# Optimization experiments

Hardware: AMD Instinct MI355X
Metric: run time of the kernel (lower is better)

Reference implementation:

```python
import jax, jax.numpy as jnp
import numpy as np

B, T, C = 8, 4096, 192
HIMG, WIMG = 64, 64
NH, HS = 24, 8
MIX_DIM, DECAY_DIM = 32, 64


def _conv2d(x, w, pad):
    # x: [B, C, H, W], w: [Cout, Cin, kh, kw]
    return jax.lax.conv_general_dilated(
        x, w, (1, 1), [(pad, pad), (pad, pad)],
        dimension_numbers=('NCHW', 'OIHW', 'NCHW'))


def setup_inputs() -> dict:
    key = jax.random.key(0)
    ks = jax.random.split(key, 26)
    f = jax.random.normal
    s = 1.0 / np.sqrt(C)
    return {
        'x': f(ks[0], (B, T, C), jnp.float32),
        'maa_x': f(ks[1], (1, 1, C), jnp.float32) * 0.1,
        'maa_w': f(ks[2], (1, 1, C), jnp.float32) * 0.1,
        'maa_k': f(ks[3], (1, 1, C), jnp.float32) * 0.1,
        'maa_v': f(ks[4], (1, 1, C), jnp.float32) * 0.1,
        'maa_r': f(ks[5], (1, 1, C), jnp.float32) * 0.1,
        'maa_g': f(ks[6], (1, 1, C), jnp.float32) * 0.1,
        'maa_w1': f(ks[7], (C, 5 * MIX_DIM), jnp.float32) * 0.01,
        'maa_w2': f(ks[8], (5, MIX_DIM, C), jnp.float32) * 0.01,
        'decay_w1': f(ks[9], (C, DECAY_DIM), jnp.float32) * 0.01,
        'decay_w2': f(ks[10], (DECAY_DIM, C), jnp.float32) * 0.01,
        'spatial_decay': f(ks[11], (1, 1, C), jnp.float32) * 0.5,
        'u': f(ks[12], (NH, HS), jnp.float32) * 0.5,
        'Wr': f(ks[13], (C, C), jnp.float32) * s,
        'Wk': f(ks[14], (C, C), jnp.float32) * s,
        'Wv': f(ks[15], (C, C), jnp.float32) * s,
        'Wg': f(ks[16], (C, C), jnp.float32) * s,
        'Wo': f(ks[17], (C, C), jnp.float32) * s,
        'ln_g': jnp.ones((C,), jnp.float32),
        'ln_b': jnp.zeros((C,), jnp.float32),
        'w_lp': f(ks[18], (C, C), jnp.float32) * s,
        'w_hd': f(ks[19], (C, C, 3), jnp.float32) * s,
        'w_vd': f(ks[20], (C, C, 3), jnp.float32) * s,
        'w_cd': f(ks[21], (C, C, 3, 3), jnp.float32) * (s / 3.0),
        'theta_cd': jnp.full((1,), 0.7, jnp.float32),
    }


def _diff_conv_mix(x2d, w_lp, w_hd, w_vd, w_cd, theta_cd):
    Cc = x2d.shape[1]
    # laplacian-pattern conv from a 1x1 weight (Conv2d_lp)
    k9 = jnp.zeros((Cc, Cc, 9), x2d.dtype)
    k9 = k9.at[:, :, jnp.array([1, 3, 5, 7])].set(w_lp[:, :, None])
    k9 = k9.at[:, :, 4].set(-4.0 * w_lp)
    out = _conv2d(x2d, k9.reshape(Cc, Cc, 3, 3), 1)
    # horizontal difference conv (Conv2d_hd)
    k9 = jnp.zeros((Cc, Cc, 9), x2d.dtype)
    k9 = k9.at[:, :, jnp.array([0, 3, 6])].set(w_hd)
    k9 = k9.at[:, :, jnp.array([2, 5, 8])].set(-w_hd)
    out = out + _conv2d(x2d, k9.reshape(Cc, Cc, 3, 3), 1)
    # vertical difference conv (Conv2d_vd)
    k9 = jnp.zeros((Cc, Cc, 9), x2d.dtype)
    k9 = k9.at[:, :, jnp.array([0, 1, 2])].set(w_vd)
    k9 = k9.at[:, :, jnp.array([6, 7, 8])].set(-w_vd)
    out = out + _conv2d(x2d, k9.reshape(Cc, Cc, 3, 3), 1)
    # central difference conv (Conv2d_cd): normal conv + 1x1 (-theta * kernel sum)
    out = out + _conv2d(x2d, w_cd, 1)
    kd = jnp.sum(w_cd, axis=(2, 3), keepdims=True) * (-theta_cd[0])
    out = out + _conv2d(x2d, kd, 0)
    return out


def reference(x, maa_x, maa_w, maa_k, maa_v, maa_r, maa_g, maa_w1, maa_w2,
              decay_w1, decay_w2, spatial_decay, u, Wr, Wk, Wv, Wg, Wo,
              ln_g, ln_b, w_lp, w_hd, w_vd, w_cd, theta_cd):
    Bb, Tt, Cc = x.shape
    x2d = x.transpose(0, 2, 1).reshape(Bb, Cc, HIMG, WIMG)
    shifted = _diff_conv_mix(x2d, w_lp, w_hd, w_vd, w_cd, theta_cd)
    xx = shifted.reshape(Bb, Cc, Tt).transpose(0, 2, 1) - x  # spatial shift delta

    # data-dependent token mixing (RWKV6 maa)
    xxx = x + xx * maa_x
    tmp = jnp.tanh(xxx @ maa_w1).reshape(Bb, Tt, 5, MIX_DIM)
    m = jnp.einsum('btfd,fdc->fbtc', tmp, maa_w2)  # [5, B, T, C]
    mw, mk, mv, mr, mg = m[0], m[1], m[2], m[3], m[4]
    xw = x + xx * (maa_w + mw)
    xk = x + xx * (maa_k + mk)
    xv = x + xx * (maa_v + mv)
    xr = x + xx * (maa_r + mr)
    xg = x + xx * (maa_g + mg)

    r = xr @ Wr
    k = xk @ Wk
    v = xv @ Wv
    g = jax.nn.silu(xg @ Wg)
    w = spatial_decay + jnp.tanh(xw @ decay_w1) @ decay_w2  # [B, T, C]

    # WKV6 linear recurrence, fp32 state, per-head [HS, HS]
    rh = r.reshape(Bb, Tt, NH, HS).astype(jnp.float32)
    kh = k.reshape(Bb, Tt, NH, HS).astype(jnp.float32)
    vh = v.reshape(Bb, Tt, NH, HS).astype(jnp.float32)
    dh = jnp.exp(-jnp.exp(w.astype(jnp.float32))).reshape(Bb, Tt, NH, HS)
    uf = u.astype(jnp.float32)

    def step(S, inp):  # S: [B, NH, HS(j key), HS(i value)]
        rt, kt, vt, dt = inp  # each [B, NH, HS]
        kv = kt[..., :, None] * vt[..., None, :]
        yt = jnp.einsum('bhj,bhji->bhi', rt, S + uf[None, :, :, None] * kv)
        return dt[..., None] * S + kv, yt

    xs = tuple(a.transpose(1, 0, 2, 3) for a in (rh, kh, vh, dh))  # time-major
    S0 = jnp.zeros((Bb, NH, HS, HS), jnp.float32)
    _, ys = jax.lax.scan(step, S0, xs)
    y = ys.transpose(1, 0, 2, 3).reshape(Bb, Tt, Cc).astype(x.dtype)

    # ln_x then gated output projection
    mu = jnp.mean(y, axis=-1, keepdims=True)
    var = jnp.mean((y - mu) ** 2, axis=-1, keepdims=True)
    yn = (y - mu) * jax.lax.rsqrt(var + 1e-5) * ln_g + ln_b
    return (yn * g) @ Wo
```

## Files before the change

### kernel.cpp

```cpp
#include <hip/hip_runtime.h>
#include <hip/hip_bf16.h>

#define Bq 8
#define Tq 4096
#define Cq 192
#define NHq 24
#define HSq 8
#define Mq (Bq * Tq)

#define CLq 64
#define NCHq (Tq / CLq)
#define TSq 32

typedef short short8 __attribute__((ext_vector_type(8)));
typedef float f32x4 __attribute__((ext_vector_type(4)));

__device__ __forceinline__ unsigned short f2bf(float f) {
    union { float f; unsigned u; } v; v.f = f;
    unsigned u = v.u;
    return (unsigned short)((u + 0x7FFFu + ((u >> 16) & 1u)) >> 16);
}
__device__ __forceinline__ float bf2f(unsigned short u) {
    union { unsigned u; float f; } v; v.u = (unsigned)u << 16;
    return v.f;
}
__device__ __forceinline__ float4 bf4_to_f4(ushort4 u) {
    return make_float4(bf2f(u.x), bf2f(u.y), bf2f(u.z), bf2f(u.w));
}

__global__ void prep_weights_kernel(const float* __restrict__ w_lp,
                                    const float* __restrict__ w_hd,
                                    const float* __restrict__ w_vd,
                                    const float* __restrict__ w_cd,
                                    const float* __restrict__ theta,
                                    unsigned short* __restrict__ Wg) {
    int idx = blockIdx.x * 256 + threadIdx.x;
    if (idx >= Cq * Cq) return;
    int cout = idx / Cq, cin = idx - cout * Cq;
    float t9[9];
#pragma unroll
    for (int t = 0; t < 9; ++t) t9[t] = 0.f;
    float lp = w_lp[idx];
    t9[1] += lp; t9[3] += lp; t9[5] += lp; t9[7] += lp; t9[4] -= 4.f * lp;
    float h0 = w_hd[idx * 3 + 0], h1 = w_hd[idx * 3 + 1], h2 = w_hd[idx * 3 + 2];
    t9[0] += h0; t9[3] += h1; t9[6] += h2;
    t9[2] -= h0; t9[5] -= h1; t9[8] -= h2;
    float v0 = w_vd[idx * 3 + 0], v1 = w_vd[idx * 3 + 1], v2 = w_vd[idx * 3 + 2];
    t9[0] += v0; t9[1] += v1; t9[2] += v2;
    t9[6] -= v0; t9[7] -= v1; t9[8] -= v2;
    float sum = 0.f;
#pragma unroll
    for (int t = 0; t < 9; ++t) {
        float cdv = w_cd[idx * 9 + t];
        t9[t] += cdv; sum += cdv;
    }
    t9[4] -= theta[0] * sum;
#pragma unroll
    for (int t = 0; t < 9; ++t)
        Wg[(size_t)cout * 1728 + t * Cq + cin] = f2bf(t9[t]);
}

__global__ void wtrans_kernel(const float* __restrict__ W,
                              unsigned short* __restrict__ Wt, int K, int N) {
    int idx = blockIdx.x * 256 + threadIdx.x;
    if (idx >= N * K) return;
    int n = idx / K, k = idx - n * K;
    Wt[idx] = f2bf(W[(size_t)k * N + n]);
}

__global__ void w2t_kernel(const float* __restrict__ w2,
                           unsigned short* __restrict__ w2t) {
    int idx = blockIdx.x * 256 + threadIdx.x;
    if (idx >= 5 * 192 * 32) return;
    int f = idx / (192 * 32), rem = idx - f * 192 * 32;
    int n = rem >> 5, k = rem & 31;
    w2t[idx] = f2bf(w2[(size_t)(f * 32 + k) * Cq + n]);
}

__global__ __launch_bounds__(256) void halo_kernel(
    const float* __restrict__ x, unsigned short* __restrict__ xh) {
    int idx = blockIdx.x * 256 + threadIdx.x;
    int c4 = (idx % 48) * 4;
    int cell = idx / 48;
    int hx = cell % 66;
    int rest = cell / 66;
    int hy = rest % 66;
    int bb = rest / 66;
    ushort4 o = make_ushort4(0, 0, 0, 0);
    if (hy >= 1 && hy <= 64 && hx >= 1 && hx <= 64) {
        size_t g = ((size_t)(bb << 12) + (hy - 1) * 64 + (hx - 1)) * Cq + c4;
        float4 v = *(const float4*)&x[g];
        o = make_ushort4(f2bf(v.x), f2bf(v.y), f2bf(v.z), f2bf(v.w));
    }
    *(ushort4*)&xh[(size_t)cell * Cq + c4] = o;
}

#define GBM 128
#define GBN 64
#define GBK 64

template <int ALOAD, int EPI, int OBF16>
__global__ __launch_bounds__(256) void mgemm_kernel(
    const unsigned short* __restrict__ Asrc,
    const unsigned short* __restrict__ Wt,
    void* __restrict__ Cv, int N, int K,
    const float* __restrict__ aux0,
    const unsigned short* __restrict__ xh,
    unsigned short* __restrict__ C2) {
    __shared__ unsigned char lds[(GBM + GBN) * GBK * 2];
    unsigned char* Alds = lds;
    unsigned char* Blds = lds + GBM * GBK * 2;
    float* C = (float*)Cv;
    unsigned short* Cb = (unsigned short*)Cv;

    const int tid = threadIdx.x;
    const int wid = tid >> 6, lane = tid & 63;
    const int llo = lane & 15, lhi = lane >> 4;
    const int m0 = blockIdx.x * GBM, n0 = blockIdx.y * GBN;

    f32x4 acc[2][4];
#pragma unroll
    for (int a = 0; a < 2; ++a)
#pragma unroll
        for (int b = 0; b < 4; ++b) {
            f32x4 z = {0.f, 0.f, 0.f, 0.f};
            acc[a][b] = z;
        }

    for (int k0 = 0; k0 < K; k0 += GBK) {
        __syncthreads();
#pragma unroll
        for (int rep = 0; rep < 4; ++rep) {
            int c = tid + rep * 256;
            int row = c >> 3, kseg = c & 7;
            int m = m0 + row;
            short8 val;
            if (ALOAD == 3) {
                val = *(const short8*)&Asrc[(size_t)m * K + k0 + kseg * 8];
            } else {
                int tap = k0 / Cq;
                int cinb = k0 - tap * Cq;
                int t3 = tap / 3;
                int bb = m >> 12, pos = m & 4095;
                int hy = (pos >> 6) + t3;
                int hx = (pos & 63) + tap - t3 * 3;
                size_t g = ((size_t)bb * 4356 + hy * 66 + hx) * Cq + cinb + kseg * 8;
                val = *(const short8*)&Asrc[g];
            }
            *(short8*)(Alds + row * 128 + ((kseg * 16) ^ ((row & 7) << 4))) = val;
        }
#pragma unroll
        for (int rep = 0; rep < 2; ++rep) {
            int c = tid + rep * 256;
            int row = c >> 3, kseg = c & 7;
            int n = n0 + row;
            short8 val = {0, 0, 0, 0, 0, 0, 0, 0};
            if (n < N) val = *(const short8*)&Wt[(size_t)n * K + k0 + kseg * 8];
            *(short8*)(Blds + row * 128 + ((kseg * 16) ^ ((row & 7) << 4))) = val;
        }
        __syncthreads();
#pragma unroll
        for (int kc = 0; kc < 2; ++kc) {
            int kb = kc * 64 + lhi * 16;
            short8 af[2], bq[4];
#pragma unroll
            for (int mf = 0; mf < 2; ++mf) {
                int row = wid * 32 + mf * 16 + llo;
                af[mf] = *(const short8*)(Alds + row * 128 + (kb ^ ((row & 7) << 4)));
            }
#pragma unroll
            for (int nf = 0; nf < 4; ++nf) {
                int row = nf * 16 + llo;
                bq[nf] = *(const short8*)(Blds + row * 128 + (kb ^ ((row & 7) << 4)));
            }
#pragma unroll
            for (int mf = 0; mf < 2; ++mf)
#pragma unroll
                for (int nf = 0; nf < 4; ++nf)
                    acc[mf][nf] = __builtin_amdgcn_mfma_f32_16x16x32_bf16(
                        af[mf], bq[nf], acc[mf][nf], 0, 0, 0);
        }
    }
    if (EPI == 5) {
#pragma unroll
        for (int mf = 0; mf < 2; ++mf)
#pragma unroll
            for (int nf = 0; nf < 4; ++nf) {
                int n = n0 + nf * 16 + llo;
#pragma unroll
                for (int r = 0; r < 4; ++r) {
                    int m = m0 + wid * 32 + mf * 16 + lhi * 4 + r;
                    int pos = m & 4095, bb = m >> 12;
                    size_t cell = (size_t)bb * 4356 + ((pos >> 6) + 1) * 66 + (pos & 63) + 1;
                    float xv = bf2f(xh[cell * Cq + n]);
                    float xxv = acc[mf][nf][r] - xv;
                    Cb[(size_t)m * Cq + n] = f2bf(xxv);
                    C2[(size_t)m * Cq + n] = f2bf(fmaf(xxv, aux0[n], xv));
                }
            }
        return;
    }
#pragma unroll
    for (int mf = 0; mf < 2; ++mf) {
#pragma unroll
        for (int nf = 0; nf < 4; ++nf) {
            int n = n0 + nf * 16 + llo;
            if (n >= N) continue;
#pragma unroll
            for (int r = 0; r < 4; ++r) {
                int m = m0 + wid * 32 + mf * 16 + lhi * 4 + r;
                float val = acc[mf][nf][r];
                if (EPI == 2) val = tanhf(val);
                else if (EPI == 3) val = val / (1.f + expf(-val));
                else if (EPI == 4) val = expf(-expf(aux0[n] + val));
                if (OBF16) Cb[(size_t)m * N + n] = f2bf(val);
                else C[(size_t)m * N + n] = val;
            }
        }
    }
}

__global__ __launch_bounds__(128) void mix5_kernel(
    const unsigned short* __restrict__ xh,
    const unsigned short* __restrict__ xxb,
    const unsigned short* __restrict__ tmp_bf,
    const unsigned short* __restrict__ w2t,
    const float* __restrict__ maa_w, const float* __restrict__ maa_k,
    const float* __restrict__ maa_v, const float* __restrict__ maa_r,
    const float* __restrict__ maa_g,
    unsigned short* __restrict__ xw, unsigned short* __restrict__ xr,
    unsigned short* __restrict__ xk, unsigned short* __restrict__ xv,
    unsigned short* __restrict__ xg) {
    const int tid = threadIdx.x;
    const int wid = tid >> 6, lane = tid & 63;
    const int llo = lane & 15, lhi = lane >> 4;
    const int mb = blockIdx.x * 64 + wid * 32;
    const int nb = blockIdx.y * 64;

    short8 aw[5][4];
#pragma unroll
    for (int f = 0; f < 5; ++f)
#pragma unroll
        for (int nf = 0; nf < 4; ++nf)
            aw[f][nf] = *(const short8*)&w2t[((size_t)f * Cq + nb + nf * 16 + llo) * 32 + lhi * 8];

#pragma unroll
    for (int sub = 0; sub < 2; ++sub) {
        short8 bt[5];
        {
            const unsigned short* trow = &tmp_bf[(size_t)(mb + sub * 16 + llo) * 160 + lhi * 8];
#pragma unroll
            for (int f = 0; f < 5; ++f) bt[f] = *(const short8*)&trow[f * 32];
        }
        int m = mb + sub * 16 + llo;
        int pos = m & 4095, bb = m >> 12;
        size_t xbase = ((size_t)bb * 4356 + ((pos >> 6) + 1) * 66 + (pos & 63) + 1) * Cq;
#pragma unroll
        for (int nf = 0; nf < 4; ++nf) {
            f32x4 acc[5];
#pragma unroll
            for (int f = 0; f < 5; ++f) {
                f32x4 z = {0.f, 0.f, 0.f, 0.f};
                acc[f] = __builtin_amdgcn_mfma_f32_16x16x32_bf16(aw[f][nf], bt[f], z, 0, 0, 0);
            }
            int n0 = nb + nf * 16 + lhi * 4;
            size_t g = (size_t)m * Cq + n0;
            float4 xv4 = bf4_to_f4(*(const ushort4*)&xh[xbase + n0]);
            float4 xx4 = bf4_to_f4(*(const ushort4*)&xxb[g]);
            float4 mw4 = *(const float4*)&maa_w[n0];
            float4 mk4 = *(const float4*)&maa_k[n0];
            float4 mv4 = *(const float4*)&maa_v[n0];
            float4 mr4 = *(const float4*)&maa_r[n0];
            float4 mg4 = *(const float4*)&maa_g[n0];
            float xvv[4] = {xv4.x, xv4.y, xv4.z, xv4.w};
            float xxv[4] = {xx4.x, xx4.y, xx4.z, xx4.w};
            float mwv[4] = {mw4.x, mw4.y, mw4.z, mw4.w};
            float mkv[4] = {mk4.x, mk4.y, mk4.z, mk4.w};
            float mvv[4] = {mv4.x, mv4.y, mv4.z, mv4.w};
            float mrv[4] = {mr4.x, mr4.y, mr4.z, mr4.w};
            float mgv[4] = {mg4.x, mg4.y, mg4.z, mg4.w};
            ushort4 ow, ok, ov, orr, og;
            unsigned short* owp = (unsigned short*)&ow;
            unsigned short* okp = (unsigned short*)&ok;
            unsigned short* ovp = (unsigned short*)&ov;
            unsigned short* orp = (unsigned short*)&orr;
            unsigned short* ogp = (unsigned short*)&og;
#pragma unroll
            for (int r = 0; r < 4; ++r) {
                owp[r] = f2bf(fmaf(xxv[r], mwv[r] + acc[0][r], xvv[r]));
                okp[r] = f2bf(fmaf(xxv[r], mkv[r] + acc[1][r], xvv[r]));
                ovp[r] = f2bf(fmaf(xxv[r], mvv[r] + acc[2][r], xvv[r]));
                orp[r] = f2bf(fmaf(xxv[r], mrv[r] + acc[3][r], xvv[r]));
                ogp[r] = f2bf(fmaf(xxv[r], mgv[r] + acc[4][r], xvv[r]));
            }
            *(ushort4*)&xw[g] = ow;
            *(ushort4*)&xk[g] = ok;
            *(ushort4*)&xv[g] = ov;
            *(ushort4*)&xr[g] = orr;
            *(ushort4*)&xg[g] = og;
        }
    }
}

__global__ __launch_bounds__(64) void wkv_pass1_kernel(
    const unsigned short* __restrict__ k, const unsigned short* __restrict__ v,
    const float* __restrict__ d,
    float* __restrict__ Dbuf, float* __restrict__ Cbuf) {
    int chunk = blockIdx.x, hg = blockIdx.y, b = blockIdx.z;
    int lane = threadIdx.x;
    int slot = lane >> 3, i = lane & 7;
    int cbase = hg * 64;
    size_t gbase = ((size_t)b * Tq + (size_t)chunk * CLq) * Cq + cbase;
    __shared__ float ks[TSq][64], vs[TSq][64], ds[TSq][64];
    float S[8], D[8];
#pragma unroll
    for (int j = 0; j < 8; ++j) { S[j] = 0.f; D[j] = 1.f; }
    for (int t0 = 0; t0 < CLq; t0 += TSq) {
        int f = lane & 15, r4 = lane >> 4;
#pragma unroll
        for (int p = 0; p < 8; ++p) {
            int row = r4 + p * 4;
            size_t g = gbase + (size_t)(t0 + row) * Cq + f * 4;
            *(float4*)&ks[row][f * 4] = bf4_to_f4(*(const ushort4*)&k[g]);
            *(float4*)&vs[row][f * 4] = bf4_to_f4(*(const ushort4*)&v[g]);
            *(float4*)&ds[row][f * 4] = *(const float4*)&d[g];
        }
        __syncthreads();
#pragma unroll 8
        for (int t = 0; t < TSq; ++t) {
            float vv = vs[t][lane];
            float4 ka = *(const float4*)&ks[t][slot * 8];
            float4 kb = *(const float4*)&ks[t][slot * 8 + 4];
            float4 da = *(const float4*)&ds[t][slot * 8];
            float4 db = *(const float4*)&ds[t][slot * 8 + 4];
            float kk[8] = {ka.x, ka.y, ka.z, ka.w, kb.x, kb.y, kb.z, kb.w};
            float dd[8] = {da.x, da.y, da.z, da.w, db.x, db.y, db.z, db.w};
#pragma unroll
            for (int j = 0; j < 8; ++j) {
                float kv = kk[j] * vv;
                S[j] = fmaf(dd[j], S[j], kv);
                D[j] *= dd[j];
            }
        }
        __syncthreads();
    }
    size_t dbase = (((size_t)b * NCHq + chunk) * NHq + hg * 8) * 8;
    Dbuf[dbase + lane] = D[i];
    size_t cb = (((size_t)b * NCHq + chunk) * NHq + (hg * 8 + slot)) * 64 + i;
#pragma unroll
    for (int j = 0; j < 8; ++j) Cbuf[cb + j * 8] = S[j];
}

__global__ __launch_bounds__(64) void wkv_pass2_kernel(
    const float* __restrict__ Dbuf, const float* __restrict__ Cbuf,
    float* __restrict__ Sbuf) {
    int bh = blockIdx.x;
    int lane = threadIdx.x;
    int j = lane >> 3, i = lane & 7;
    int b = bh / NHq, h = bh - b * NHq;
    float S = 0.f;
    size_t stride = (size_t)NHq * 64;
    size_t base = ((size_t)b * NCHq * NHq + h) * 64 + j * 8 + i;
    size_t dstride = (size_t)NHq * 8;
    size_t dbase = ((size_t)b * NCHq * NHq + h) * 8 + j;
#pragma unroll 4
    for (int c = 0; c < NCHq; ++c) {
        Sbuf[base + c * stride] = S;
        float D = Dbuf[dbase + c * dstride];
        float C = Cbuf[base + c * stride];
        S = fmaf(D, S, C);
    }
}

__global__ __launch_bounds__(64) void wkv_pass3_kernel(
    const unsigned short* __restrict__ r, const unsigned short* __restrict__ k,
    const unsigned short* __restrict__ v, const float* __restrict__ d,
    const float* __restrict__ u, const float* __restrict__ Sbuf,
    unsigned short* __restrict__ y) {
    int chunk = blockIdx.x, hg = blockIdx.y, b = blockIdx.z;
    int lane = threadIdx.x;
    int slot = lane >> 3, i = lane & 7;
    int h = hg * 8 + slot;
    int cbase = hg * 64;
    size_t gbase = ((size_t)b * Tq + (size_t)chunk * CLq) * Cq + cbase;
    __shared__ float rs[TSq][64], ks[TSq][64], vs[TSq][64], ds[TSq][64];
    float S[8], uu[8];
    size_t sb = (((size_t)b * NCHq + chunk) * NHq + h) * 64 + i;
#pragma unroll
    for (int j = 0; j < 8; ++j) {
        S[j] = Sbuf[sb + j * 8];
        uu[j] = u[h * 8 + j];
    }
    for (int t0 = 0; t0 < CLq; t0 += TSq) {
        int f = lane & 15, r4 = lane >> 4;
#pragma unroll
        for (int p = 0; p < 8; ++p) {
            int row = r4 + p * 4;
            size_t g = gbase + (size_t)(t0 + row) * Cq + f * 4;
            *(float4*)&rs[row][f * 4] = bf4_to_f4(*(const ushort4*)&r[g]);
            *(float4*)&ks[row][f * 4] = bf4_to_f4(*(const ushort4*)&k[g]);
            *(float4*)&vs[row][f * 4] = bf4_to_f4(*(const ushort4*)&v[g]);
            *(float4*)&ds[row][f * 4] = *(const float4*)&d[g];
        }
        __syncthreads();
#pragma unroll 8
        for (int t = 0; t < TSq; ++t) {
            float vv = vs[t][lane];
            float4 ra = *(const float4*)&rs[t][slot * 8];
            float4 rb = *(const float4*)&rs[t][slot * 8 + 4];
            float4 ka = *(const float4*)&ks[t][slot * 8];
            float4 kb = *(const float4*)&ks[t][slot * 8 + 4];
            float4 da = *(const float4*)&ds[t][slot * 8];
            float4 db = *(const float4*)&ds[t][slot * 8 + 4];
            float rr[8] = {ra.x, ra.y, ra.z, ra.w, rb.x, rb.y, rb.z, rb.w};
            float kk[8] = {ka.x, ka.y, ka.z, ka.w, kb.x, kb.y, kb.z, kb.w};
            float dd[8] = {da.x, da.y, da.z, da.w, db.x, db.y, db.z, db.w};
            float yv = 0.f;
#pragma unroll
            for (int j = 0; j < 8; ++j) {
                float kv = kk[j] * vv;
                yv = fmaf(rr[j], fmaf(uu[j], kv, S[j]), yv);
                S[j] = fmaf(dd[j], S[j], kv);
            }
            y[gbase + (size_t)(t0 + t) * Cq + lane] = f2bf(yv);
        }
        __syncthreads();
    }
}

__global__ __launch_bounds__(256) void ln_gate_kernel(
    const unsigned short* __restrict__ y, const unsigned short* __restrict__ g,
    const float* __restrict__ ln_g, const float* __restrict__ ln_b,
    unsigned short* __restrict__ out) {
    int row = blockIdx.x * 4 + (threadIdx.x >> 6);
    int lane = threadIdx.x & 63;
    const unsigned short* yr = y + (size_t)row * Cq;
    float a0 = bf2f(yr[lane]), a1 = bf2f(yr[lane + 64]), a2 = bf2f(yr[lane + 128]);
    float s = a0 + a1 + a2;
    float ss = a0 * a0 + a1 * a1 + a2 * a2;
#pragma unroll
    for (int m = 1; m < 64; m <<= 1) {
        s += __shfl_xor(s, m);
        ss += __shfl_xor(ss, m);
    }
    float mu = s * (1.f / 192.f);
    float var = ss * (1.f / 192.f) - mu * mu;
    float rstd = rsqrtf(var + 1e-5f);
    const unsigned short* gr = g + (size_t)row * Cq;
    unsigned short* orow = out + (size_t)row * Cq;
    float aa[3] = {a0, a1, a2};
#pragma unroll
    for (int q = 0; q < 3; ++q) {
        int cc = lane + q * 64;
        float yn = (aa[q] - mu) * rstd * ln_g[cc] + ln_b[cc];
        orow[cc] = f2bf(yn * bf2f(gr[cc]));
    }
}

extern "C" void kernel_launch(void* const* d_in, const int* in_sizes, int n_in,
                              void* d_out, int out_size, void* d_ws, size_t ws_size,
                              hipStream_t stream) {
    const float* x        = (const float*)d_in[0];
    const float* maa_x    = (const float*)d_in[1];
    const float* maa_w    = (const float*)d_in[2];
    const float* maa_k    = (const float*)d_in[3];
    const float* maa_v    = (const float*)d_in[4];
    const float* maa_r    = (const float*)d_in[5];
    const float* maa_g    = (const float*)d_in[6];
    const float* maa_w1   = (const float*)d_in[7];
    const float* maa_w2   = (const float*)d_in[8];
    const float* decay_w1 = (const float*)d_in[9];
    const float* decay_w2 = (const float*)d_in[10];
    const float* sdecay   = (const float*)d_in[11];
    const float* u        = (const float*)d_in[12];
    const float* Wr       = (const float*)d_in[13];
    const float* Wk       = (const float*)d_in[14];
    const float* Wv       = (const float*)d_in[15];
    const float* Wgp      = (const float*)d_in[16];
    const float* Wo       = (const float*)d_in[17];
    const float* ln_g     = (const float*)d_in[18];
    const float* ln_b     = (const float*)d_in[19];
    const float* w_lp     = (const float*)d_in[20];
    const float* w_hd     = (const float*)d_in[21];
    const float* w_vd     = (const float*)d_in[22];
    const float* w_cd     = (const float*)d_in[23];
    const float* theta    = (const float*)d_in[24];
    float* out = (float*)d_out;

    const size_t BIG = (size_t)Mq * Cq;
    float* ws = (float*)d_ws;
    unsigned short* Wgt_conv = (unsigned short*)ws;
    unsigned short* Wt_maa = Wgt_conv + (size_t)Cq * 1728;
    unsigned short* Wt_r = Wt_maa + 160 * Cq;
    unsigned short* Wt_k = Wt_r + Cq * Cq;
    unsigned short* Wt_v = Wt_k + Cq * Cq;
    unsigned short* Wt_g = Wt_v + Cq * Cq;
    unsigned short* Wt_o = Wt_g + Cq * Cq;
    unsigned short* w2t  = Wt_o + Cq * Cq;
    unsigned short* Wt_d1 = w2t + 5 * 192 * 32;
    unsigned short* Wt_d2 = Wt_d1 + 64 * Cq;
    float* tmp  = ws + 331776;
    float* wtmp = tmp + (size_t)Mq * 160;
    float* buf0 = wtmp + (size_t)Mq * 64;
    float* buf1 = buf0 + BIG;
    float* buf2 = buf1 + BIG;
    float* buf3 = buf2 + BIG;
    float* buf4 = buf3 + BIG;
    float* buf5 = buf4 + BIG;

    unsigned short* tmp_bf = (unsigned short*)tmp;
    float* Dbuf = tmp + (size_t)Mq * 80;
    float* Cbuf = Dbuf + (size_t)Bq * NCHq * NHq * 8;
    float* Sbuf = Cbuf + (size_t)Bq * NCHq * NHq * 64;

    unsigned short* x_halo = (unsigned short*)buf1;
    unsigned short* y_b    = (unsigned short*)buf1;
    unsigned short* xx_b   = (unsigned short*)buf0;
    unsigned short* xw_b   = (unsigned short*)(buf0 + BIG / 2);
    unsigned short* r_b    = (unsigned short*)buf0;
    unsigned short* xxx_b  = (unsigned short*)(buf2 + BIG / 2);
    unsigned short* xg_b   = xxx_b;
    unsigned short* xv_b   = (unsigned short*)buf2;
    unsigned short* k_b    = (unsigned short*)buf2;
    unsigned short* gate_b = (unsigned short*)buf2;
    unsigned short* v_b    = (unsigned short*)buf3;
    unsigned short* g_b    = (unsigned short*)buf4;
    unsigned short* xr_b   = (unsigned short*)buf5;
    unsigned short* xk_b   = (unsigned short*)(buf5 + BIG / 2);
    float* d_f             = buf5;
    unsigned short* wtmp_b = (unsigned short*)wtmp;

    dim3 blk(256);
    dim3 mg(Mq / GBM, 3);
    const unsigned short* nosrc = nullptr;
    unsigned short* nodst = nullptr;

    prep_weights_kernel<<<dim3(144), blk, 0, stream>>>(w_lp, w_hd, w_vd, w_cd, theta, Wgt_conv);
    wtrans_kernel<<<dim3(120), blk, 0, stream>>>(maa_w1, Wt_maa, Cq, 160);
    wtrans_kernel<<<dim3(144), blk, 0, stream>>>(Wr, Wt_r, Cq, Cq);
    wtrans_kernel<<<dim3(144), blk, 0, stream>>>(Wk, Wt_k, Cq, Cq);
    wtrans_kernel<<<dim3(144), blk, 0, stream>>>(Wv, Wt_v, Cq, Cq);
    wtrans_kernel<<<dim3(144), blk, 0, stream>>>(Wgp, Wt_g, Cq, Cq);
    wtrans_kernel<<<dim3(144), blk, 0, stream>>>(Wo, Wt_o, Cq, Cq);
    w2t_kernel<<<dim3(120), blk, 0, stream>>>(maa_w2, w2t);
    wtrans_kernel<<<dim3(48), blk, 0, stream>>>(decay_w1, Wt_d1, Cq, 64);
    wtrans_kernel<<<dim3(48), blk, 0, stream>>>(decay_w2, Wt_d2, 64, Cq);
    halo_kernel<<<dim3(8 * 66 * 66 * 48 / 256), blk, 0, stream>>>(x, x_halo);
    mgemm_kernel<1, 5, 1><<<mg, blk, 0, stream>>>(x_halo, Wgt_conv, xx_b, Cq, 1728, maa_x, x_halo, xxx_b);
    mgemm_kernel<3, 2, 1><<<mg, blk, 0, stream>>>(xxx_b, Wt_maa, tmp_bf, 160, Cq, nullptr, nosrc, nodst);
    mix5_kernel<<<dim3(Mq / 64, 3), dim3(128), 0, stream>>>(
        x_halo, xx_b, tmp_bf, w2t, maa_w, maa_k, maa_v, maa_r, maa_g,
        xw_b, xr_b, xk_b, xv_b, xg_b);
    mgemm_kernel<3, 0, 1><<<mg, blk, 0, stream>>>(xv_b, Wt_v, v_b, Cq, Cq, nullptr, nosrc, nodst);
    mgemm_kernel<3, 3, 1><<<mg, blk, 0, stream>>>(xg_b, Wt_g, g_b, Cq, Cq, nullptr, nosrc, nodst);
    mgemm_kernel<3, 0, 1><<<mg, blk, 0, stream>>>(xr_b, Wt_r, r_b, Cq, Cq, nullptr, nosrc, nodst);
    mgemm_kernel<3, 0, 1><<<mg, blk, 0, stream>>>(xk_b, Wt_k, k_b, Cq, Cq, nullptr, nosrc, nodst);
    mgemm_kernel<3, 2, 1><<<dim3(Mq / GBM, 1), blk, 0, stream>>>(xw_b, Wt_d1, wtmp_b, 64, Cq, nullptr, nosrc, nodst);
    mgemm_kernel<3, 4, 0><<<mg, blk, 0, stream>>>(wtmp_b, Wt_d2, d_f, Cq, 64, sdecay, nosrc, nodst);
    wkv_pass1_kernel<<<dim3(NCHq, 3, Bq), dim3(64), 0, stream>>>(k_b, v_b, d_f, Dbuf, Cbuf);
    wkv_pass2_kernel<<<dim3(Bq * NHq), dim3(64), 0, stream>>>(Dbuf, Cbuf, Sbuf);
    wkv_pass3_kernel<<<dim3(NCHq, 3, Bq), dim3(64), 0, stream>>>(r_b, k_b, v_b, d_f, u, Sbuf, y_b);
    ln_gate_kernel<<<dim3(Mq / 4), blk, 0, stream>>>(y_b, g_b, ln_g, ln_b, gate_b);
    mgemm_kernel<3, 0, 0><<<mg, blk, 0, stream>>>(gate_b, Wt_o, out, Cq, Cq, nullptr, nosrc, nodst);
}
```

Before: 359.7 us.

## Batch weight packing, merge four projection GEMMs, widen conv GEMM tile, stage mix5 stores

Nine weight-transpose launches become one prep_pack kernel, and the four r/k/v/g projection GEMMs become a single proj4 launch that uses blockIdx.z, applying SiLU only for the gate. The conv GEMM now takes a templated N-tile of 96, so the A operand built from the halo is loaded twice per row block instead of three times. mix5 stages its outputs through LDS so global writes become full 16-byte rows. k_b moves to a separate buffer so it no longer aliases inputs of the fused projection. These changes target launch overhead, redundant im2col A traffic and narrow stores, at the cost of more LDS and registers per block.

```diff
diff --git a/kernel.cpp b/kernel.cpp
--- a/kernel.cpp
+++ b/kernel.cpp
@@ -60,21 +60,50 @@
         Wg[(size_t)cout * 1728 + t * Cq + cin] = f2bf(t9[t]);
 }
 
-__global__ void wtrans_kernel(const float* __restrict__ W,
-                              unsigned short* __restrict__ Wt, int K, int N) {
+__global__ __launch_bounds__(256) void prep_pack_kernel(
+    const float* __restrict__ maa_w1, const float* __restrict__ Wr,
+    const float* __restrict__ Wk, const float* __restrict__ Wv,
+    const float* __restrict__ Wgp, const float* __restrict__ Wo,
+    const float* __restrict__ maa_w2, const float* __restrict__ d1,
+    const float* __restrict__ d2,
+    unsigned short* __restrict__ Wt_maa, unsigned short* __restrict__ Wt_r,
+    unsigned short* __restrict__ Wt_k, unsigned short* __restrict__ Wt_v,
+    unsigned short* __restrict__ Wt_g, unsigned short* __restrict__ Wt_o,
+    unsigned short* __restrict__ w2t, unsigned short* __restrict__ Wt_d1,
+    unsigned short* __restrict__ Wt_d2) {
     int idx = blockIdx.x * 256 + threadIdx.x;
-    if (idx >= N * K) return;
-    int n = idx / K, k = idx - n * K;
-    Wt[idx] = f2bf(W[(size_t)k * N + n]);
-}
-
-__global__ void w2t_kernel(const float* __restrict__ w2,
-                           unsigned short* __restrict__ w2t) {
-    int idx = blockIdx.x * 256 + threadIdx.x;
-    if (idx >= 5 * 192 * 32) return;
-    int f = idx / (192 * 32), rem = idx - f * 192 * 32;
-    int n = rem >> 5, k = rem & 31;
-    w2t[idx] = f2bf(w2[(size_t)(f * 32 + k) * Cq + n]);
+    if (idx < 30720) {
+        int n = idx / 192, k = idx - n * 192;
+        Wt_maa[idx] = f2bf(maa_w1[(size_t)k * 160 + n]);
+        return;
+    }
+    idx -= 30720;
+    if (idx < 5 * 36864) {
+        int s = idx / 36864, e = idx - s * 36864;
+        int n = e / 192, k = e - n * 192;
+        const float* W = s == 0 ? Wr : s == 1 ? Wk : s == 2 ? Wv : s == 3 ? Wgp : Wo;
+        unsigned short* D = s == 0 ? Wt_r : s == 1 ? Wt_k : s == 2 ? Wt_v : s == 3 ? Wt_g : Wt_o;
+        D[e] = f2bf(W[(size_t)k * 192 + n]);
+        return;
+    }
+    idx -= 5 * 36864;
+    if (idx < 30720) {
+        int f = idx / 6144, rem = idx - f * 6144;
+        int n = rem >> 5, k = rem & 31;
+        w2t[idx] = f2bf(maa_w2[(size_t)(f * 32 + k) * 192 + n]);
+        return;
+    }
+    idx -= 30720;
+    if (idx < 12288) {
+        int n = idx / 192, k = idx - n * 192;
+        Wt_d1[idx] = f2bf(d1[(size_t)k * 64 + n]);
+        return;
+    }
+    idx -= 12288;
+    if (idx < 12288) {
+        int n = idx / 64, k = idx - n * 64;
+        Wt_d2[idx] = f2bf(d2[(size_t)k * 192 + n]);
+    }
 }
 
 __global__ __launch_bounds__(256) void halo_kernel(
@@ -96,10 +125,9 @@
 }
 
 #define GBM 128
-#define GBN 64
 #define GBK 64
 
-template <int ALOAD, int EPI, int OBF16>
+template <int ALOAD, int EPI, int OBF16, int BN>
 __global__ __launch_bounds__(256) void mgemm_kernel(
     const unsigned short* __restrict__ Asrc,
     const unsigned short* __restrict__ Wt,
@@ -107,7 +135,7 @@
     const float* __restrict__ aux0,
     const unsigned short* __restrict__ xh,
     unsigned short* __restrict__ C2) {
-    __shared__ unsigned char lds[(GBM + GBN) * GBK * 2];
+    __shared__ unsigned char lds[(GBM + BN) * GBK * 2];
     unsigned char* Alds = lds;
     unsigned char* Blds = lds + GBM * GBK * 2;
     float* C = (float*)Cv;
@@ -116,13 +144,14 @@
     const int tid = threadIdx.x;
     const int wid = tid >> 6, lane = tid & 63;
     const int llo = lane & 15, lhi = lane >> 4;
-    const int m0 = blockIdx.x * GBM, n0 = blockIdx.y * GBN;
-
-    f32x4 acc[2][4];
+    const int m0 = blockIdx.x * GBM, n0 = blockIdx.y * BN;
+    const int NF = BN / 16;
+
+    f32x4 acc[2][BN / 16];
 #pragma unroll
     for (int a = 0; a < 2; ++a)
 #pragma unroll
-        for (int b = 0; b < 4; ++b) {
+        for (int b = 0; b < NF; ++b) {
             f32x4 z = {0.f, 0.f, 0.f, 0.f};
             acc[a][b] = z;
         }
@@ -150,7 +179,7 @@
             *(short8*)(Alds + row * 128 + ((kseg * 16) ^ ((row & 7) << 4))) = val;
         }
 #pragma unroll
-        for (int rep = 0; rep < 2; ++rep) {
+        for (int rep = 0; rep < BN / 32; ++rep) {
             int c = tid + rep * 256;
             int row = c >> 3, kseg = c & 7;
             int n = n0 + row;
@@ -162,21 +191,21 @@
 #pragma unroll
         for (int kc = 0; kc < 2; ++kc) {
             int kb = kc * 64 + lhi * 16;
-            short8 af[2], bq[4];
+            short8 af[2], bq[BN / 16];
 #pragma unroll
             for (int mf = 0; mf < 2; ++mf) {
                 int row = wid * 32 + mf * 16 + llo;
                 af[mf] = *(const short8*)(Alds + row * 128 + (kb ^ ((row & 7) << 4)));
             }
 #pragma unroll
-            for (int nf = 0; nf < 4; ++nf) {
+            for (int nf = 0; nf < NF; ++nf) {
                 int row = nf * 16 + llo;
                 bq[nf] = *(const short8*)(Blds + row * 128 + (kb ^ ((row & 7) << 4)));
             }
 #pragma unroll
             for (int mf = 0; mf < 2; ++mf)
 #pragma unroll
-                for (int nf = 0; nf < 4; ++nf)
+                for (int nf = 0; nf < NF; ++nf)
                     acc[mf][nf] = __builtin_amdgcn_mfma_f32_16x16x32_bf16(
                         af[mf], bq[nf], acc[mf][nf], 0, 0, 0);
         }
@@ -185,7 +214,7 @@
 #pragma unroll
         for (int mf = 0; mf < 2; ++mf)
 #pragma unroll
-            for (int nf = 0; nf < 4; ++nf) {
+            for (int nf = 0; nf < NF; ++nf) {
                 int n = n0 + nf * 16 + llo;
 #pragma unroll
                 for (int r = 0; r < 4; ++r) {
@@ -203,7 +232,7 @@
 #pragma unroll
     for (int mf = 0; mf < 2; ++mf) {
 #pragma unroll
-        for (int nf = 0; nf < 4; ++nf) {
+        for (int nf = 0; nf < NF; ++nf) {
             int n = n0 + nf * 16 + llo;
             if (n >= N) continue;
 #pragma unroll
@@ -211,7 +240,6 @@
                 int m = m0 + wid * 32 + mf * 16 + lhi * 4 + r;
                 float val = acc[mf][nf][r];
                 if (EPI == 2) val = tanhf(val);
-                else if (EPI == 3) val = val / (1.f + expf(-val));
                 else if (EPI == 4) val = expf(-expf(aux0[n] + val));
                 if (OBF16) Cb[(size_t)m * N + n] = f2bf(val);
                 else C[(size_t)m * N + n] = val;
@@ -220,6 +248,91 @@
     }
 }
 
+__global__ __launch_bounds__(256) void proj4_kernel(
+    const unsigned short* __restrict__ A0, const unsigned short* __restrict__ A1,
+    const unsigned short* __restrict__ A2, const unsigned short* __restrict__ A3,
+    const unsigned short* __restrict__ W0, const unsigned short* __restrict__ W1,
+    const unsigned short* __restrict__ W2, const unsigned short* __restrict__ W3,
+    unsigned short* __restrict__ O0, unsigned short* __restrict__ O1,
+    unsigned short* __restrict__ O2, unsigned short* __restrict__ O3) {
+    __shared__ unsigned char lds[(GBM + 64) * GBK * 2];
+    unsigned char* Alds = lds;
+    unsigned char* Blds = lds + GBM * GBK * 2;
+    const int z = blockIdx.z;
+    const unsigned short* Asrc = z == 0 ? A0 : z == 1 ? A1 : z == 2 ? A2 : A3;
+    const unsigned short* Wt = z == 0 ? W0 : z == 1 ? W1 : z == 2 ? W2 : W3;
+    unsigned short* Cb = z == 0 ? O0 : z == 1 ? O1 : z == 2 ? O2 : O3;
+    const bool silu = (z == 3);
+
+    const int tid = threadIdx.x;
+    const int wid = tid >> 6, lane = tid & 63;
+    const int llo = lane & 15, lhi = lane >> 4;
+    const int m0 = blockIdx.x * GBM, n0 = blockIdx.y * 64;
+
+    f32x4 acc[2][4];
+#pragma unroll
+    for (int a = 0; a < 2; ++a)
+#pragma unroll
+        for (int b = 0; b < 4; ++b) {
+            f32x4 zz = {0.f, 0.f, 0.f, 0.f};
+            acc[a][b] = zz;
+        }
+
+    for (int k0 = 0; k0 < Cq; k0 += GBK) {
+        __syncthreads();
+#pragma unroll
+        for (int rep = 0; rep < 4; ++rep) {
+            int c = tid + rep * 256;
+            int row = c >> 3, kseg = c & 7;
+            short8 val = *(const short8*)&Asrc[(size_t)(m0 + row) * Cq + k0 + kseg * 8];
+            *(short8*)(Alds + row * 128 + ((kseg * 16) ^ ((row & 7) << 4))) = val;
+        }
+#pragma unroll
+        for (int rep = 0; rep < 2; ++rep) {
+            int c = tid + rep * 256;
+            int row = c >> 3, kseg = c & 7;
+            short8 val = *(const short8*)&Wt[(size_t)(n0 + row) * Cq + k0 + kseg * 8];
+            *(short8*)(Blds + row * 128 + ((kseg * 16) ^ ((row & 7) << 4))) = val;
+        }
+        __syncthreads();
+#pragma unroll
+        for (int kc = 0; kc < 2; ++kc) {
+            int kb = kc * 64 + lhi * 16;
+            short8 af[2], bq[4];
+#pragma unroll
+            for (int mf = 0; mf < 2; ++mf) {
+                int row = wid * 32 + mf * 16 + llo;
+                af[mf] = *(const short8*)(Alds + row * 128 + (kb ^ ((row & 7) << 4)));
+            }
+#pragma unroll
+            for (int nf = 0; nf < 4; ++nf) {
+                int row = nf * 16 + llo;
+                bq[nf] = *(const short8*)(Blds + row * 128 + (kb ^ ((row & 7) << 4)));
+            }
+#pragma unroll
+            for (int mf = 0; mf < 2; ++mf)
+#pragma unroll
+                for (int nf = 0; nf < 4; ++nf)
+                    acc[mf][nf] = __builtin_amdgcn_mfma_f32_16x16x32_bf16(
+                        af[mf], bq[nf], acc[mf][nf], 0, 0, 0);
+        }
+    }
+#pragma unroll
+    for (int mf = 0; mf < 2; ++mf)
+#pragma unroll
+        for (int nf = 0; nf < 4; ++nf) {
+            int n = n0 + nf * 16 + llo;
+#pragma unroll
+            for (int r = 0; r < 4; ++r) {
+                int m = m0 + wid * 32 + mf * 16 + lhi * 4 + r;
+                float val = acc[mf][nf][r];
+                if (silu) val = val / (1.f + expf(-val));
+                Cb[(size_t)m * Cq + n] = f2bf(val);
+            }
+        }
+}
+
+#define MLDW 72
 __global__ __launch_bounds__(128) void mix5_kernel(
     const unsigned short* __restrict__ xh,
     const unsigned short* __restrict__ xxb,
@@ -231,6 +344,7 @@
     unsigned short* __restrict__ xw, unsigned short* __restrict__ xr,
     unsigned short* __restrict__ xk, unsigned short* __restrict__ xv,
     unsigned short* __restrict__ xg) {
+    __shared__ unsigned short tile[2][5][16][MLDW];
     const int tid = threadIdx.x;
     const int wid = tid >> 6, lane = tid & 63;
     const int llo = lane & 15, lhi = lane >> 4;
@@ -243,6 +357,8 @@
 #pragma unroll
         for (int nf = 0; nf < 4; ++nf)
             aw[f][nf] = *(const short8*)&w2t[((size_t)f * Cq + nb + nf * 16 + llo) * 32 + lhi * 8];
+
+    unsigned short* const outs[5] = {xw, xk, xv, xr, xg};
 
 #pragma unroll
     for (int sub = 0; sub < 2; ++sub) {
@@ -279,25 +395,31 @@
             float mvv[4] = {mv4.x, mv4.y, mv4.z, mv4.w};
             float mrv[4] = {mr4.x, mr4.y, mr4.z, mr4.w};
             float mgv[4] = {mg4.x, mg4.y, mg4.z, mg4.w};
-            ushort4 ow, ok, ov, orr, og;
-            unsigned short* owp = (unsigned short*)&ow;
-            unsigned short* okp = (unsigned short*)&ok;
-            unsigned short* ovp = (unsigned short*)&ov;
-            unsigned short* orp = (unsigned short*)&orr;
-            unsigned short* ogp = (unsigned short*)&og;
+            ushort4 ov[5];
 #pragma unroll
             for (int r = 0; r < 4; ++r) {
-                owp[r] = f2bf(fmaf(xxv[r], mwv[r] + acc[0][r], xvv[r]));
-                okp[r] = f2bf(fmaf(xxv[r], mkv[r] + acc[1][r], xvv[r]));
-                ovp[r] = f2bf(fmaf(xxv[r], mvv[r] + acc[2][r], xvv[r]));
-                orp[r] = f2bf(fmaf(xxv[r], mrv[r] + acc[3][r], xvv[r]));
-                ogp[r] = f2bf(fmaf(xxv[r], mgv[r] + acc[4][r], xvv[r]));
-            }
-            *(ushort4*)&xw[g] = ow;
-            *(ushort4*)&xk[g] = ok;
-            *(ushort4*)&xv[g] = ov;
-            *(ushort4*)&xr[g] = orr;
-            *(ushort4*)&xg[g] = og;
+                ((unsigned short*)&ov[0])[r] = f2bf(fmaf(xxv[r], mwv[r] + acc[0][r], xvv[r]));
+                ((unsigned short*)&ov[1])[r] = f2bf(fmaf(xxv[r], mkv[r] + acc[1][r], xvv[r]));
+                ((unsigned short*)&ov[2])[r] = f2bf(fmaf(xxv[r], mvv[r] + acc[2][r], xvv[r]));
+                ((unsigned short*)&ov[3])[r] = f2bf(fmaf(xxv[r], mrv[r] + acc[3][r], xvv[r]));
+                ((unsigned short*)&ov[4])[r] = f2bf(fmaf(xxv[r], mgv[r] + acc[4][r], xvv[r]));
+            }
+            int col = nf * 16 + lhi * 4;
+#pragma unroll
+            for (int f = 0; f < 5; ++f)
+                *(ushort4*)&tile[wid][f][llo][col] = ov[f];
+        }
+        int row16 = lane >> 3;
+        int colc = (lane & 7) * 8;
+#pragma unroll
+        for (int f = 0; f < 5; ++f) {
+#pragma unroll
+            for (int p = 0; p < 2; ++p) {
+                int rr = p * 8 + row16;
+                int gm = mb + sub * 16 + rr;
+                *(short8*)&outs[f][(size_t)gm * Cq + nb + colc] =
+                    *(const short8*)&tile[wid][f][rr][colc];
+            }
         }
     }
 }
@@ -515,13 +637,13 @@
 
     unsigned short* x_halo = (unsigned short*)buf1;
     unsigned short* y_b    = (unsigned short*)buf1;
+    unsigned short* k_b    = (unsigned short*)(buf1 + BIG / 2);
     unsigned short* xx_b   = (unsigned short*)buf0;
     unsigned short* xw_b   = (unsigned short*)(buf0 + BIG / 2);
     unsigned short* r_b    = (unsigned short*)buf0;
     unsigned short* xxx_b  = (unsigned short*)(buf2 + BIG / 2);
     unsigned short* xg_b   = xxx_b;
     unsigned short* xv_b   = (unsigned short*)buf2;
-    unsigned short* k_b    = (unsigned short*)buf2;
     unsigned short* gate_b = (unsigned short*)buf2;
     unsigned short* v_b    = (unsigned short*)buf3;
     unsigned short* g_b    = (unsigned short*)buf4;
@@ -531,35 +653,33 @@
     unsigned short* wtmp_b = (unsigned short*)wtmp;
 
     dim3 blk(256);
-    dim3 mg(Mq / GBM, 3);
     const unsigned short* nosrc = nullptr;
     unsigned short* nodst = nullptr;
 
     prep_weights_kernel<<<dim3(144), blk, 0, stream>>>(w_lp, w_hd, w_vd, w_cd, theta, Wgt_conv);
-    wtrans_kernel<<<dim3(120), blk, 0, stream>>>(maa_w1, Wt_maa, Cq, 160);
-    wtrans_kernel<<<dim3(144), blk, 0, stream>>>(Wr, Wt_r, Cq, Cq);
-    wtrans_kernel<<<dim3(144), blk, 0, stream>>>(Wk, Wt_k, Cq, Cq);
-    wtrans_kernel<<<dim3(144), blk, 0, stream>>>(Wv, Wt_v, Cq, Cq);
-    wtrans_kernel<<<dim3(144), blk, 0, stream>>>(Wgp, Wt_g, Cq, Cq);
-    wtrans_kernel<<<dim3(144), blk, 0, stream>>>(Wo, Wt_o, Cq, Cq);
-    w2t_kernel<<<dim3(120), blk, 0, stream>>>(maa_w2, w2t);
-    wtrans_kernel<<<dim3(48), blk, 0, stream>>>(decay_w1, Wt_d1, Cq, 64);
-    wtrans_kernel<<<dim3(48), blk, 0, stream>>>(decay_w2, Wt_d2, 64, Cq);
+    prep_pack_kernel<<<dim3(1056), blk, 0, stream>>>(
+        maa_w1, Wr, Wk, Wv, Wgp, Wo, maa_w2, decay_w1, decay_w2,
+        Wt_maa, Wt_r, Wt_k, Wt_v, Wt_g, Wt_o, w2t, Wt_d1, Wt_d2);
     halo_kernel<<<dim3(8 * 66 * 66 * 48 / 256), blk, 0, stream>>>(x, x_halo);
-    mgemm_kernel<1, 5, 1><<<mg, blk, 0, stream>>>(x_halo, Wgt_conv, xx_b, Cq, 1728, maa_x, x_halo, xxx_b);
-    mgemm_kernel<3, 2, 1><<<mg, blk, 0, stream>>>(xxx_b, Wt_maa, tmp_bf, 160, Cq, nullptr, nosrc, nodst);
+    mgemm_kernel<1, 5, 1, 96><<<dim3(Mq / GBM, 2), blk, 0, stream>>>(
+        x_halo, Wgt_conv, xx_b, Cq, 1728, maa_x, x_halo, xxx_b);
+    mgemm_kernel<3, 2, 1, 64><<<dim3(Mq / GBM, 3), blk, 0, stream>>>(
+        xxx_b, Wt_maa, tmp_bf, 160, Cq, nullptr, nosrc, nodst);
     mix5_kernel<<<dim3(Mq / 64, 3), dim3(128), 0, stream>>>(
         x_halo, xx_b, tmp_bf, w2t, maa_w, maa_k, maa_v, maa_r, maa_g,
         xw_b, xr_b, xk_b, xv_b, xg_b);
-    mgemm_kernel<3, 0, 1><<<mg, blk, 0, stream>>>(xv_b, Wt_v, v_b, Cq, Cq, nullptr, nosrc, nodst);
-    mgemm_kernel<3, 3, 1><<<mg, blk, 0, stream>>>(xg_b, Wt_g, g_b, Cq, Cq, nullptr, nosrc, nodst);
-    mgemm_kernel<3, 0, 1><<<mg, blk, 0, stream>>>(xr_b, Wt_r, r_b, Cq, Cq, nullptr, nosrc, nodst);
-    mgemm_kernel<3, 0, 1><<<mg, blk, 0, stream>>>(xk_b, Wt_k, k_b, Cq, Cq, nullptr, nosrc, nodst);
-    mgemm_kernel<3, 2, 1><<<dim3(Mq / GBM, 1), blk, 0, stream>>>(xw_b, Wt_d1, wtmp_b, 64, Cq, nullptr, nosrc, nodst);
-    mgemm_kernel<3, 4, 0><<<mg, blk, 0, stream>>>(wtmp_b, Wt_d2, d_f, Cq, 64, sdecay, nosrc, nodst);
+    proj4_kernel<<<dim3(Mq / GBM, 3, 4), blk, 0, stream>>>(
+        xv_b, xr_b, xk_b, xg_b,
+        Wt_v, Wt_r, Wt_k, Wt_g,
+        v_b, r_b, k_b, g_b);
+    mgemm_kernel<3, 2, 1, 64><<<dim3(Mq / GBM, 1), blk, 0, stream>>>(
+        xw_b, Wt_d1, wtmp_b, 64, Cq, nullptr, nosrc, nodst);
+    mgemm_kernel<3, 4, 0, 64><<<dim3(Mq / GBM, 3), blk, 0, stream>>>(
+        wtmp_b, Wt_d2, d_f, Cq, 64, sdecay, nosrc, nodst);
     wkv_pass1_kernel<<<dim3(NCHq, 3, Bq), dim3(64), 0, stream>>>(k_b, v_b, d_f, Dbuf, Cbuf);
     wkv_pass2_kernel<<<dim3(Bq * NHq), dim3(64), 0, stream>>>(Dbuf, Cbuf, Sbuf);
     wkv_pass3_kernel<<<dim3(NCHq, 3, Bq), dim3(64), 0, stream>>>(r_b, k_b, v_b, d_f, u, Sbuf, y_b);
     ln_gate_kernel<<<dim3(Mq / 4), blk, 0, stream>>>(y_b, g_b, ln_g, ln_b, gate_b);
-    mgemm_kernel<3, 0, 0><<<mg, blk, 0, stream>>>(gate_b, Wt_o, out, Cq, Cq, nullptr, nosrc, nodst);
-}
+    mgemm_kernel<3, 0, 0, 64><<<dim3(Mq / GBM, 3), blk, 0, stream>>>(
+        gate_b, Wt_o, out, Cq, Cq, nullptr, nosrc, nodst);
+}
```

New measurement: 329.1 us. 1.09x faster.
